# Optimization experiments

Hardware: AMD Instinct MI355X
Metric: run time of the kernel (lower is better)

The kernel has to match this reference:

```python
import jax, jax.numpy as jnp
import numpy as np

B, T, D, H, NW = 2, 2048, 1024, 16, 64
HD = D // H  # 64
EPS = 1e-12  # F.normalize eps


def setup_inputs() -> dict:
    key = jax.random.key(0)
    ks = jax.random.split(key, 8)
    def lin(k, din, dout):
        return jax.random.normal(k, (din, dout), jnp.float32) / np.sqrt(din).astype(np.float32)
    return {
        "x": jax.random.normal(ks[0], (B, T, D), jnp.float32),
        "Wqf": lin(ks[1], D, H * NW), "bqf": jnp.zeros((H * NW,), jnp.float32),
        "Wkf": lin(ks[2], D, H * NW), "bkf": jnp.zeros((H * NW,), jnp.float32),
        "Wqp": lin(ks[3], D, H * NW), "bqp": jnp.zeros((H * NW,), jnp.float32),
        "Wkp": lin(ks[4], D, H * NW), "bkp": jnp.zeros((H * NW,), jnp.float32),
        "Wv": lin(ks[5], D, D), "bv": jnp.zeros((D,), jnp.float32),
        "Wo": lin(ks[6], D, D), "bo": jnp.zeros((D,), jnp.float32),
        "scale": jnp.ones((H, 1, 1), jnp.float32),  # interference_scale
    }


def reference(x, Wqf, bqf, Wkf, bkf, Wqp, bqp, Wkp, bkp, Wv, bv, Wo, bo, scale):
    Bx, Tx, Dx = x.shape
    def heads(W, b, nd):  # [B,T,H*nd] -> [B,H,T,nd]
        return jnp.transpose((x @ W + b).reshape(Bx, Tx, H, nd), (0, 2, 1, 3))
    qf = heads(Wqf, bqf, NW); kf = heads(Wkf, bkf, NW)
    qp = heads(Wqp, bqp, NW); kp = heads(Wkp, bkp, NW)
    v = heads(Wv, bv, HD)
    t = jnp.arange(Tx, dtype=x.dtype)[None, None, :, None]  # [1,1,T,1]
    def wave_norm(f, p):
        w = jnp.sin(f * t + p)  # [B,H,T,NW]
        n = jnp.sqrt(jnp.sum(w * w, axis=-1, keepdims=True))
        return w / jnp.maximum(n, EPS)
    qn = wave_norm(qf, qp)
    kn = wave_norm(kf, kp)
    inter = jnp.einsum('bhtw,bhsw->bhts', qn, kn) * scale[None]  # [B,H,T,T]
    causal = jnp.tril(jnp.ones((Tx, Tx), bool))  # keep diag and below
    inter = jnp.where(causal, inter, jnp.zeros((), x.dtype))
    denom = jnp.sqrt(jnp.arange(1, Tx + 1, dtype=x.dtype))[:, None]  # [T,1]
    attn = inter / denom
    # dropout is identity in eval mode
    out = jnp.einsum('bhts,bhsd->bhtd', attn, v)
    out = jnp.transpose(out, (0, 2, 1, 3)).reshape(Bx, Tx, Dx)
    return out @ Wo + bo
```

## Files before the change

### kernel.cpp

```cpp
#include <hip/hip_runtime.h>


#define Bb 2
#define Tt 2048
#define Dd 1024
#define Hh 16
#define NC 32

typedef _Float16 half_t;
typedef _Float16 half8 __attribute__((ext_vector_type(8)));
typedef _Float16 half4h __attribute__((ext_vector_type(4)));
typedef float float4v __attribute__((ext_vector_type(4)));
typedef float f32x16 __attribute__((ext_vector_type(16)));

#define MFMA16(a, b, c) __builtin_amdgcn_mfma_f32_16x16x32_f16((a), (b), (c), 0, 0, 0)
#define MFMA32(a, b, c) __builtin_amdgcn_mfma_f32_32x32x16_f16((a), (b), (c), 0, 0, 0)

#define LOADREGS(K)                                                       \
  rg0 = *(const half8*)&srcHi[(K)];      rg1 = *(const half8*)&srcHi[(K) + 8];  \
  rg2 = *(const half8*)&srcHi[(K) + 16]; rg3 = *(const half8*)&srcHi[(K) + 24]; \
  rg4 = *(const half8*)&srcLo[(K)];      rg5 = *(const half8*)&srcLo[(K) + 8];  \
  rg6 = *(const half8*)&srcLo[(K) + 16]; rg7 = *(const half8*)&srcLo[(K) + 24];

#define WRITEREGS(BI) {                                                   \
  half_t* d_ = dstRow + (BI) * 8192;                                      \
  *(half8*)&d_[pc0] = rg0; *(half8*)&d_[pc1] = rg1;                       \
  *(half8*)&d_[pc2] = rg2; *(half8*)&d_[pc3] = rg3;                       \
  *(half8*)&d_[pc4] = rg4; *(half8*)&d_[pc5] = rg5;                       \
  *(half8*)&d_[pc6] = rg6; *(half8*)&d_[pc7] = rg7; }

#define KTILE_MFMA(BI)                                                    \
  _Pragma("unroll")                                                       \
  for (int ks = 0; ks < 2; ++ks) {                                        \
    half8 ahi = *(const half8*)&As[BI][32 * w + rl][((2 * ks + kq) ^ sw) * 8];       \
    half8 alo = *(const half8*)&As[BI][32 * w + rl][((4 + 2 * ks + kq) ^ sw) * 8];   \
    _Pragma("unroll")                                                     \
    for (int tn = 0; tn < 4; ++tn) {                                      \
      half8 bhi = *(const half8*)&Bs[BI][32 * tn + rl][((2 * ks + kq) ^ sw) * 8];    \
      half8 blo = *(const half8*)&Bs[BI][32 * tn + rl][((4 + 2 * ks + kq) ^ sw) * 8];\
      hh[tn] = MFMA32(ahi, bhi, hh[tn]);                                  \
      mx[tn] = MFMA32(ahi, blo, mx[tn]);                                  \
      mx[tn] = MFMA32(alo, bhi, mx[tn]);                                  \
    }                                                                     \
  }

__global__ __launch_bounds__(256) void xsplit_kernel(
    const float* __restrict__ X, half_t* __restrict__ XHI, half_t* __restrict__ XLO)
{
  const size_t i = ((size_t)blockIdx.x * 256 + threadIdx.x) * 8;
  float4 a = *(const float4*)&X[i];
  float4 b = *(const float4*)&X[i + 4];
  const float av[8] = {a.x, a.y, a.z, a.w, b.x, b.y, b.z, b.w};
  half8 hv, lv;
  #pragma unroll
  for (int j = 0; j < 8; ++j) {
    half_t hx = (half_t)av[j];
    hv[j] = hx; lv[j] = (half_t)((av[j] - (float)hx) * 2048.f);
  }
  *(half8*)&XHI[i] = hv;
  *(half8*)&XLO[i] = lv;
}

__global__ __launch_bounds__(256) void wsplit_kernel(
    const float* __restrict__ W0, const float* __restrict__ W1,
    const float* __restrict__ W2, const float* __restrict__ W3,
    const float* __restrict__ W4, const float* __restrict__ W5,
    half_t* __restrict__ WSP)
{
  __shared__ float Ld[64][68];
  const int tid = threadIdx.x;
  const int m = blockIdx.z;
  const float* W = (m == 0) ? W0 : (m == 1) ? W1 : (m == 2) ? W2
                 : (m == 3) ? W3 : (m == 4) ? W4 : W5;
  const int k0 = blockIdx.x * 64, n0 = blockIdx.y * 64;
  const int r = tid >> 2, c4 = (tid & 3) * 16;
  #pragma unroll
  for (int i = 0; i < 4; ++i)
    *(float4*)&Ld[r][c4 + i * 4] =
        *(const float4*)&W[(size_t)(k0 + r) * Dd + n0 + c4 + i * 4];
  __syncthreads();
  half_t* hi = WSP + (size_t)m * 2097152;
  half_t* lo = hi + 1048576;
  const int n = tid >> 2, kc = (tid & 3) * 16;
  half8 hv0, hv1, lv0, lv1;
  #pragma unroll
  for (int i = 0; i < 8; ++i) {
    float v0 = Ld[kc + i][n];
    half_t h0 = (half_t)v0;
    hv0[i] = h0; lv0[i] = (half_t)((v0 - (float)h0) * 2048.f);
    float v1 = Ld[kc + 8 + i][n];
    half_t h1 = (half_t)v1;
    hv1[i] = h1; lv1[i] = (half_t)((v1 - (float)h1) * 2048.f);
  }
  *(half8*)&hi[(size_t)(n0 + n) * Dd + k0 + kc]     = hv0;
  *(half8*)&hi[(size_t)(n0 + n) * Dd + k0 + kc + 8] = hv1;
  *(half8*)&lo[(size_t)(n0 + n) * Dd + k0 + kc]     = lv0;
  *(half8*)&lo[(size_t)(n0 + n) * Dd + k0 + kc + 8] = lv1;
}

__global__ __launch_bounds__(256, 2) void proj_kernel(
    const half_t* __restrict__ XHI, const half_t* __restrict__ XLO,
    const half_t* __restrict__ WSP,
    const float* __restrict__ bqf, const float* __restrict__ bqp,
    const float* __restrict__ bkf, const float* __restrict__ bkp,
    half_t* __restrict__ QNH, half_t* __restrict__ KNH)
{
  __shared__ __align__(16) half_t As[2][128][64];
  __shared__ __align__(16) half_t Bs[2][128][64];
  const int tid = threadIdx.x;
  const int mb = blockIdx.x, h = blockIdx.y;
  const int b = blockIdx.z >> 1, p = blockIdx.z & 1;
  const int t0 = mb * 128, row0 = b * Tt + t0, col0 = h * 64;
  const half_t* WF = WSP + (size_t)(2 * p) * 2097152;
  const half_t* WP = WSP + (size_t)(2 * p + 1) * 2097152;
  const float* BF = p ? bkf : bqf;
  const float* BP = p ? bkp : bqp;
  half_t* OUTH = p ? KNH : QNH;

  f32x16 hh[4], mx[4];
  #pragma unroll
  for (int i = 0; i < 4; ++i) { hh[i] = (f32x16)(0.f); mx[i] = (f32x16)(0.f); }

  const int lane = tid & 63, w = tid >> 6;
  const int rl = lane & 31, kq = lane >> 5;
  const int sw = rl & 7;

  const int r = tid & 127, isB = tid >> 7;
  const int swr = r & 7;
  const half_t* srcHi;
  const half_t* srcLo;
  if (!isB) {
    srcHi = &XHI[(size_t)(row0 + r) * Dd];
    srcLo = &XLO[(size_t)(row0 + r) * Dd];
  } else {
    const half_t* Wb = (r < 64) ? (WF + (size_t)(col0 + r) * Dd)
                                : (WP + (size_t)(col0 + r - 64) * Dd);
    srcHi = Wb; srcLo = Wb + 1048576;
  }
  half_t* dstRow = isB ? &Bs[0][r][0] : &As[0][r][0];
  const int pc0 = ((0 ^ swr)) * 8, pc1 = ((1 ^ swr)) * 8;
  const int pc2 = ((2 ^ swr)) * 8, pc3 = ((3 ^ swr)) * 8;
  const int pc4 = ((4 ^ swr)) * 8, pc5 = ((5 ^ swr)) * 8;
  const int pc6 = ((6 ^ swr)) * 8, pc7 = ((7 ^ swr)) * 8;

  half8 rg0, rg1, rg2, rg3, rg4, rg5, rg6, rg7;
  LOADREGS(0)
  WRITEREGS(0)
  LOADREGS(32)
  __syncthreads();

  #pragma unroll 1
  for (int k0 = 0; k0 < Dd; k0 += 64) {
    KTILE_MFMA(0)
    WRITEREGS(1)
    if (k0 + 64 < Dd) { LOADREGS(k0 + 64) }
    __syncthreads();
    KTILE_MFMA(1)
    if (k0 + 64 < Dd) { WRITEREGS(0) }
    if (k0 + 96 < Dd) { LOADREGS(k0 + 96) }
    __syncthreads();
  }

  const float bf0 = BF[col0 + rl], bf1 = BF[col0 + 32 + rl];
  const float bp0 = BP[col0 + rl], bp1 = BP[col0 + 32 + rl];
  #pragma unroll
  for (int j = 0; j < 16; ++j) {
    const int rt = (j & 3) + 8 * (j >> 2) + 4 * kq;
    const float tf = (float)(t0 + 32 * w + rt);
    float f0 = hh[0][j] + mx[0][j] * (1.f / 2048.f) + bf0;
    float f1 = hh[1][j] + mx[1][j] * (1.f / 2048.f) + bf1;
    float p0 = hh[2][j] + mx[2][j] * (1.f / 2048.f) + bp0;
    float p1 = hh[3][j] + mx[3][j] * (1.f / 2048.f) + bp1;
    float w0 = sinf(fmaf(f0, tf, p0));
    float w1 = sinf(fmaf(f1, tf, p1));
    float ss = w0 * w0 + w1 * w1;
    ss += __shfl_xor(ss, 1); ss += __shfl_xor(ss, 2);
    ss += __shfl_xor(ss, 4); ss += __shfl_xor(ss, 8);
    ss += __shfl_xor(ss, 16);
    const float inv = 1.f / fmaxf(sqrtf(ss), 1e-12f);
    half_t* op = &OUTH[((size_t)(b * Tt) + t0 + 32 * w + rt) * Dd + col0];
    op[rl]      = (half_t)(w0 * inv);
    op[32 + rl] = (half_t)(w1 * inv);
  }
}

__global__ __launch_bounds__(256, 2) void gemm_kernel(
    const half_t* __restrict__ AHI, const half_t* __restrict__ ALO,
    const half_t* __restrict__ WHI,
    const float* __restrict__ BIAS, float* __restrict__ OUT)
{
  __shared__ __align__(16) half_t As[2][128][64];
  __shared__ __align__(16) half_t Bs[2][128][64];
  const int tid = threadIdx.x;
  const int m0 = blockIdx.x * 128, n0 = blockIdx.y * 128;

  f32x16 hh[4], mx[4];
  #pragma unroll
  for (int i = 0; i < 4; ++i) { hh[i] = (f32x16)(0.f); mx[i] = (f32x16)(0.f); }

  const int lane = tid & 63, w = tid >> 6;
  const int rl = lane & 31, kq = lane >> 5;
  const int sw = rl & 7;

  const int r = tid & 127, isB = tid >> 7;
  const int swr = r & 7;
  const half_t* srcHi = isB ? &WHI[(size_t)(n0 + r) * Dd]
                            : &AHI[(size_t)(m0 + r) * Dd];
  const half_t* srcLo = isB ? &WHI[1048576 + (size_t)(n0 + r) * Dd]
                            : &ALO[(size_t)(m0 + r) * Dd];
  half_t* dstRow = isB ? &Bs[0][r][0] : &As[0][r][0];
  const int pc0 = ((0 ^ swr)) * 8, pc1 = ((1 ^ swr)) * 8;
  const int pc2 = ((2 ^ swr)) * 8, pc3 = ((3 ^ swr)) * 8;
  const int pc4 = ((4 ^ swr)) * 8, pc5 = ((5 ^ swr)) * 8;
  const int pc6 = ((6 ^ swr)) * 8, pc7 = ((7 ^ swr)) * 8;

  half8 rg0, rg1, rg2, rg3, rg4, rg5, rg6, rg7;
  LOADREGS(0)
  WRITEREGS(0)
  LOADREGS(32)
  __syncthreads();

  #pragma unroll 1
  for (int k0 = 0; k0 < Dd; k0 += 64) {
    KTILE_MFMA(0)
    WRITEREGS(1)
    if (k0 + 64 < Dd) { LOADREGS(k0 + 64) }
    __syncthreads();
    KTILE_MFMA(1)
    if (k0 + 64 < Dd) { WRITEREGS(0) }
    if (k0 + 96 < Dd) { LOADREGS(k0 + 96) }
    __syncthreads();
  }

  const float bb0 = BIAS[n0 + rl],      bb1 = BIAS[n0 + 32 + rl];
  const float bb2 = BIAS[n0 + 64 + rl], bb3 = BIAS[n0 + 96 + rl];
  #pragma unroll
  for (int j = 0; j < 16; ++j) {
    const int rt = (j & 3) + 8 * (j >> 2) + 4 * kq;
    float* orow = &OUT[(size_t)(m0 + 32 * w + rt) * Dd + n0];
    orow[rl]      = hh[0][j] + mx[0][j] * (1.f / 2048.f) + bb0;
    orow[32 + rl] = hh[1][j] + mx[1][j] * (1.f / 2048.f) + bb1;
    orow[64 + rl] = hh[2][j] + mx[2][j] * (1.f / 2048.f) + bb2;
    orow[96 + rl] = hh[3][j] + mx[3][j] * (1.f / 2048.f) + bb3;
  }
}

__global__ __launch_bounds__(256) void chunk_kv_kernel(
    const half_t* __restrict__ KNH, const float* __restrict__ V,
    float* __restrict__ G)
{
  __shared__ float Ks[64][64];
  __shared__ float Vs[64][64];
  const int tid = threadIdx.x;
  const int c = blockIdx.x, h = blockIdx.y, b = blockIdx.z;
  const int s0 = c * 64;
  const int lr = tid >> 2, lc = (tid & 3) * 16;
  {
    const half_t* krow = &KNH[(size_t)(b * Tt + s0 + lr) * Dd + h * 64 + lc];
    half8 ka = *(const half8*)&krow[0];
    half8 kb = *(const half8*)&krow[8];
    #pragma unroll
    for (int i = 0; i < 8; ++i) {
      Ks[lr][lc + i] = (float)ka[i];
      Ks[lr][lc + 8 + i] = (float)kb[i];
    }
    const float* vrow = &V[(size_t)(b * Tt + s0 + lr) * Dd + h * 64 + lc];
    #pragma unroll
    for (int i = 0; i < 4; ++i)
      *(float4*)&Vs[lr][lc + i * 4] = *(const float4*)&vrow[i * 4];
  }
  __syncthreads();

  const int ty = tid >> 4, tx = tid & 15;
  float g[4][4] = {{0.f}};
  #pragma unroll 4
  for (int s = 0; s < 64; ++s) {
    float4 kv = *(const float4*)&Ks[s][ty * 4];
    float4 vv = *(const float4*)&Vs[s][tx * 4];
    const float* k_ = (const float*)&kv;
    const float* v_ = (const float*)&vv;
    #pragma unroll
    for (int i = 0; i < 4; ++i)
      #pragma unroll
      for (int j = 0; j < 4; ++j)
        g[i][j] = fmaf(k_[i], v_[j], g[i][j]);
  }
  float* Gp = G + (((size_t)(b * Hh + h) * NC + c) << 12);
  #pragma unroll
  for (int i = 0; i < 4; ++i)
    *(float4*)&Gp[(ty * 4 + i) * 64 + tx * 4] =
        make_float4(g[i][0], g[i][1], g[i][2], g[i][3]);
}

__global__ __launch_bounds__(256) void prefix_kernel(float* __restrict__ G)
{
  const int seg = blockIdx.x, h = blockIdx.y, b = blockIdx.z;
  float* base = G + (((size_t)(b * Hh + h) * NC) << 12) + seg * 256 + threadIdx.x;
  float acc = 0.f;
  #pragma unroll 4
  for (int c = 0; c < NC; ++c) {
    float* p = base + ((size_t)c << 12);
    const float g = *p;
    *p = acc;
    acc += g;
  }
}

__global__ __launch_bounds__(256) void attn_chunk_kernel(
    const half_t* __restrict__ QNH, const half_t* __restrict__ KNH,
    const float* __restrict__ V, const float* __restrict__ M,
    const float* __restrict__ SCALE,
    half_t* __restrict__ ATTHI, half_t* __restrict__ ATTLO)
{
  __shared__ float Qt[64][68];
  __shared__ float Kt[64][68];
  __shared__ float SM[64][68];
  __shared__ float Vs[64][64];
  const int tid = threadIdx.x;
  const int c = blockIdx.x, h = blockIdx.y, b = blockIdx.z;
  const int t0 = c * 64;
  const int lr = tid >> 2, lc = (tid & 3) * 16;
  {
    const half_t* qrow = &QNH[(size_t)(b * Tt + t0 + lr) * Dd + h * 64 + lc];
    const half_t* krow = &KNH[(size_t)(b * Tt + t0 + lr) * Dd + h * 64 + lc];
    half8 qa = *(const half8*)&qrow[0];
    half8 qb = *(const half8*)&qrow[8];
    half8 ka = *(const half8*)&krow[0];
    half8 kb = *(const half8*)&krow[8];
    #pragma unroll
    for (int i = 0; i < 8; ++i) {
      Qt[lc + i][lr] = (float)qa[i];     Qt[lc + 8 + i][lr] = (float)qb[i];
      Kt[lc + i][lr] = (float)ka[i];     Kt[lc + 8 + i][lr] = (float)kb[i];
    }
    const float* vrow = &V[(size_t)(b * Tt + t0 + lr) * Dd + h * 64 + lc];
    const float* mrow = &M[(((size_t)(b * Hh + h) * NC + c) << 12) + lr * 64 + lc];
    #pragma unroll
    for (int i = 0; i < 4; ++i) {
      *(float4*)&Vs[lr][lc + i * 4] = *(const float4*)&vrow[i * 4];
      *(float4*)&SM[lr][lc + i * 4] = *(const float4*)&mrow[i * 4];
    }
  }
  __syncthreads();

  const int ty = tid >> 4, tx = tid & 15;
  float o[4][4] = {{0.f}};
  float sc[4][4] = {{0.f}};

  #pragma unroll 4
  for (int w = 0; w < 64; ++w) {
    float4 qv = *(const float4*)&Qt[w][ty * 4];
    float4 mv = *(const float4*)&SM[w][tx * 4];
    float4 kv = *(const float4*)&Kt[w][tx * 4];
    const float* q_ = (const float*)&qv;
    const float* m_ = (const float*)&mv;
    const float* k_ = (const float*)&kv;
    #pragma unroll
    for (int i = 0; i < 4; ++i) {
      float qq = q_[i];
      #pragma unroll
      for (int j = 0; j < 4; ++j) {
        o[i][j]  = fmaf(qq, m_[j], o[i][j]);
        sc[i][j] = fmaf(qq, k_[j], sc[i][j]);
      }
    }
  }
  __syncthreads();

  #pragma unroll
  for (int i = 0; i < 4; ++i) {
    const int lt = ty * 4 + i;
    #pragma unroll
    for (int j = 0; j < 4; ++j) {
      const int ls = tx * 4 + j;
      SM[ls][lt] = (ls <= lt) ? sc[i][j] : 0.f;
    }
  }
  __syncthreads();

  #pragma unroll 4
  for (int s = 0; s < 64; ++s) {
    float4 sv = *(const float4*)&SM[s][ty * 4];
    float4 vv = *(const float4*)&Vs[s][tx * 4];
    const float* s_ = (const float*)&sv;
    const float* v_ = (const float*)&vv;
    #pragma unroll
    for (int i = 0; i < 4; ++i)
      #pragma unroll
      for (int j = 0; j < 4; ++j)
        o[i][j] = fmaf(s_[i], v_[j], o[i][j]);
  }

  const float sch = SCALE[h];
  #pragma unroll
  for (int i = 0; i < 4; ++i) {
    const int t = t0 + ty * 4 + i;
    const float fac = sch / sqrtf((float)(t + 1));
    half4h hv, lv;
    #pragma unroll
    for (int j = 0; j < 4; ++j) {
      float v = o[i][j] * fac;
      half_t hx = (half_t)v;
      hv[j] = hx; lv[j] = (half_t)((v - (float)hx) * 2048.f);
    }
    *(half4h*)&ATTHI[(size_t)(b * Tt + t) * Dd + h * 64 + tx * 4] = hv;
    *(half4h*)&ATTLO[(size_t)(b * Tt + t) * Dd + h * 64 + tx * 4] = lv;
  }
}

extern "C" void kernel_launch(void* const* d_in, const int* in_sizes, int n_in,
                              void* d_out, int out_size, void* d_ws, size_t ws_size,
                              hipStream_t stream) {
  const float* x   = (const float*)d_in[0];
  const float* Wqf = (const float*)d_in[1];
  const float* bqf = (const float*)d_in[2];
  const float* Wkf = (const float*)d_in[3];
  const float* bkf = (const float*)d_in[4];
  const float* Wqp = (const float*)d_in[5];
  const float* bqp = (const float*)d_in[6];
  const float* Wkp = (const float*)d_in[7];
  const float* bkp = (const float*)d_in[8];
  const float* Wv  = (const float*)d_in[9];
  const float* bv  = (const float*)d_in[10];
  const float* Wo  = (const float*)d_in[11];
  const float* bo  = (const float*)d_in[12];
  const float* scale = (const float*)d_in[13];

  half_t* WSP = (half_t*)d_ws;
  half_t* qnh = WSP + 12582912;
  half_t* knh = qnh + 4194304;
  float*  G   = (float*)(knh + 4194304);
  half_t* xhi = (half_t*)G;
  half_t* xlo = xhi + 4194304;
  float*  vbuf = (float*)d_out;

  xsplit_kernel<<<dim3(2048), 256, 0, stream>>>(x, xhi, xlo);

  wsplit_kernel<<<dim3(16, 16, 6), 256, 0, stream>>>(Wqf, Wqp, Wkf, Wkp, Wv, Wo, WSP);

  proj_kernel<<<dim3(Tt / 128, Hh, Bb * 2), 256, 0, stream>>>(
      xhi, xlo, WSP, bqf, bqp, bkf, bkp, qnh, knh);

  gemm_kernel<<<dim3((Bb * Tt) / 128, Dd / 128), 256, 0, stream>>>(
      xhi, xlo, WSP + (size_t)4 * 2097152, bv, vbuf);

  chunk_kv_kernel<<<dim3(NC, Hh, Bb), 256, 0, stream>>>(knh, vbuf, G);
  prefix_kernel<<<dim3(16, Hh, Bb), 256, 0, stream>>>(G);
  attn_chunk_kernel<<<dim3(NC, Hh, Bb), 256, 0, stream>>>(
      qnh, knh, vbuf, G, scale, qnh , knh );

  gemm_kernel<<<dim3((Bb * Tt) / 128, Dd / 128), 256, 0, stream>>>(
      qnh, knh, WSP + (size_t)5 * 2097152, bo, (float*)d_out);
}
```

Measured before the change: 367.3 us.

## Store GEMM tiles in MFMA fragment order in LDS, single-buffered 32-wide K

Replaces the swizzled row-major double-buffered LDS tiles in the projection and output GEMM kernels with separate hi/lo buffers laid out in MFMA operand-fragment order. Each lane then reads its operand with one contiguous 16-byte load and no XOR address arithmetic. The K loop now steps 32 at a time with one buffer and two barriers per step, overlapping the next global load with the MFMAs. This halves LDS per block, which may help occupancy, but doubles the number of barriers and drops the double buffering.

```diff
diff --git a/kernel.cpp b/kernel.cpp
--- a/kernel.cpp
+++ b/kernel.cpp
@@ -16,32 +16,32 @@
 #define MFMA16(a, b, c) __builtin_amdgcn_mfma_f32_16x16x32_f16((a), (b), (c), 0, 0, 0)
 #define MFMA32(a, b, c) __builtin_amdgcn_mfma_f32_32x32x16_f16((a), (b), (c), 0, 0, 0)
 
-#define LOADREGS(K)                                                       \
-  rg0 = *(const half8*)&srcHi[(K)];      rg1 = *(const half8*)&srcHi[(K) + 8];  \
-  rg2 = *(const half8*)&srcHi[(K) + 16]; rg3 = *(const half8*)&srcHi[(K) + 24]; \
-  rg4 = *(const half8*)&srcLo[(K)];      rg5 = *(const half8*)&srcLo[(K) + 8];  \
+
+#define LOADREGS(K)                                                            \
+  rg0 = *(const half8*)&srcHi[(K)];      rg1 = *(const half8*)&srcHi[(K) + 8]; \
+  rg2 = *(const half8*)&srcHi[(K) + 16]; rg3 = *(const half8*)&srcHi[(K) + 24];\
+  rg4 = *(const half8*)&srcLo[(K)];      rg5 = *(const half8*)&srcLo[(K) + 8]; \
   rg6 = *(const half8*)&srcLo[(K) + 16]; rg7 = *(const half8*)&srcLo[(K) + 24];
 
-#define WRITEREGS(BI) {                                                   \
-  half_t* d_ = dstRow + (BI) * 8192;                                      \
-  *(half8*)&d_[pc0] = rg0; *(half8*)&d_[pc1] = rg1;                       \
-  *(half8*)&d_[pc2] = rg2; *(half8*)&d_[pc3] = rg3;                       \
-  *(half8*)&d_[pc4] = rg4; *(half8*)&d_[pc5] = rg5;                       \
-  *(half8*)&d_[pc6] = rg6; *(half8*)&d_[pc7] = rg7; }
-
-#define KTILE_MFMA(BI)                                                    \
-  _Pragma("unroll")                                                       \
-  for (int ks = 0; ks < 2; ++ks) {                                        \
-    half8 ahi = *(const half8*)&As[BI][32 * w + rl][((2 * ks + kq) ^ sw) * 8];       \
-    half8 alo = *(const half8*)&As[BI][32 * w + rl][((4 + 2 * ks + kq) ^ sw) * 8];   \
-    _Pragma("unroll")                                                     \
-    for (int tn = 0; tn < 4; ++tn) {                                      \
-      half8 bhi = *(const half8*)&Bs[BI][32 * tn + rl][((2 * ks + kq) ^ sw) * 8];    \
-      half8 blo = *(const half8*)&Bs[BI][32 * tn + rl][((4 + 2 * ks + kq) ^ sw) * 8];\
-      hh[tn] = MFMA32(ahi, bhi, hh[tn]);                                  \
-      mx[tn] = MFMA32(ahi, blo, mx[tn]);                                  \
-      mx[tn] = MFMA32(alo, bhi, mx[tn]);                                  \
-    }                                                                     \
+#define WRITEFRAGS {                                                           \
+  *(half8*)&dHi[0]    = rg0;  *(half8*)&dHi[256]  = rg1;                       \
+  *(half8*)&dHi[2048] = rg2;  *(half8*)&dHi[2304] = rg3;                       \
+  *(half8*)&dLo[0]    = rg4;  *(half8*)&dLo[256]  = rg5;                       \
+  *(half8*)&dLo[2048] = rg6;  *(half8*)&dLo[2304] = rg7; }
+
+#define KTILE_MFMA                                                             \
+  _Pragma("unroll")                                                            \
+  for (int ks = 0; ks < 2; ++ks) {                                             \
+    half8 ahi = *(const half8*)&AhiF[(ks * 4 + w) * 512 + lane * 8];           \
+    half8 alo = *(const half8*)&AloF[(ks * 4 + w) * 512 + lane * 8];           \
+    _Pragma("unroll")                                                          \
+    for (int tn = 0; tn < 4; ++tn) {                                           \
+      half8 bhi = *(const half8*)&BhiF[(ks * 4 + tn) * 512 + lane * 8];        \
+      half8 blo = *(const half8*)&BloF[(ks * 4 + tn) * 512 + lane * 8];        \
+      hh[tn] = MFMA32(ahi, bhi, hh[tn]);                                       \
+      mx[tn] = MFMA32(ahi, blo, mx[tn]);                                       \
+      mx[tn] = MFMA32(alo, bhi, mx[tn]);                                       \
+    }                                                                          \
   }
 
 __global__ __launch_bounds__(256) void xsplit_kernel(
@@ -105,8 +105,10 @@
     const float* __restrict__ bkf, const float* __restrict__ bkp,
     half_t* __restrict__ QNH, half_t* __restrict__ KNH)
 {
-  __shared__ __align__(16) half_t As[2][128][64];
-  __shared__ __align__(16) half_t Bs[2][128][64];
+  __shared__ __align__(16) half_t AhiF[4096];
+  __shared__ __align__(16) half_t AloF[4096];
+  __shared__ __align__(16) half_t BhiF[4096];
+  __shared__ __align__(16) half_t BloF[4096];
   const int tid = threadIdx.x;
   const int mb = blockIdx.x, h = blockIdx.y;
   const int b = blockIdx.z >> 1, p = blockIdx.z & 1;
@@ -123,10 +125,9 @@
 
   const int lane = tid & 63, w = tid >> 6;
   const int rl = lane & 31, kq = lane >> 5;
-  const int sw = rl & 7;
 
   const int r = tid & 127, isB = tid >> 7;
-  const int swr = r & 7;
+  const int rt = r >> 5, rr = r & 31;
   const half_t* srcHi;
   const half_t* srcLo;
   if (!isB) {
@@ -137,27 +138,17 @@
                                 : (WP + (size_t)(col0 + r - 64) * Dd);
     srcHi = Wb; srcLo = Wb + 1048576;
   }
-  half_t* dstRow = isB ? &Bs[0][r][0] : &As[0][r][0];
-  const int pc0 = ((0 ^ swr)) * 8, pc1 = ((1 ^ swr)) * 8;
-  const int pc2 = ((2 ^ swr)) * 8, pc3 = ((3 ^ swr)) * 8;
-  const int pc4 = ((4 ^ swr)) * 8, pc5 = ((5 ^ swr)) * 8;
-  const int pc6 = ((6 ^ swr)) * 8, pc7 = ((7 ^ swr)) * 8;
+  half_t* dHi = (isB ? BhiF : AhiF) + rt * 512 + rr * 8;
+  half_t* dLo = (isB ? BloF : AloF) + rt * 512 + rr * 8;
 
   half8 rg0, rg1, rg2, rg3, rg4, rg5, rg6, rg7;
   LOADREGS(0)
-  WRITEREGS(0)
-  LOADREGS(32)
-  __syncthreads();
-
-  #pragma unroll 1
-  for (int k0 = 0; k0 < Dd; k0 += 64) {
-    KTILE_MFMA(0)
-    WRITEREGS(1)
-    if (k0 + 64 < Dd) { LOADREGS(k0 + 64) }
+
+  for (int k0 = 0; k0 < Dd; k0 += 32) {
+    WRITEFRAGS
     __syncthreads();
-    KTILE_MFMA(1)
-    if (k0 + 64 < Dd) { WRITEREGS(0) }
-    if (k0 + 96 < Dd) { LOADREGS(k0 + 96) }
+    if (k0 + 32 < Dd) { LOADREGS(k0 + 32) }
+    KTILE_MFMA
     __syncthreads();
   }
 
@@ -165,8 +156,8 @@
   const float bp0 = BP[col0 + rl], bp1 = BP[col0 + 32 + rl];
   #pragma unroll
   for (int j = 0; j < 16; ++j) {
-    const int rt = (j & 3) + 8 * (j >> 2) + 4 * kq;
-    const float tf = (float)(t0 + 32 * w + rt);
+    const int rtj = (j & 3) + 8 * (j >> 2) + 4 * kq;
+    const float tf = (float)(t0 + 32 * w + rtj);
     float f0 = hh[0][j] + mx[0][j] * (1.f / 2048.f) + bf0;
     float f1 = hh[1][j] + mx[1][j] * (1.f / 2048.f) + bf1;
     float p0 = hh[2][j] + mx[2][j] * (1.f / 2048.f) + bp0;
@@ -178,7 +169,7 @@
     ss += __shfl_xor(ss, 4); ss += __shfl_xor(ss, 8);
     ss += __shfl_xor(ss, 16);
     const float inv = 1.f / fmaxf(sqrtf(ss), 1e-12f);
-    half_t* op = &OUTH[((size_t)(b * Tt) + t0 + 32 * w + rt) * Dd + col0];
+    half_t* op = &OUTH[((size_t)(b * Tt) + t0 + 32 * w + rtj) * Dd + col0];
     op[rl]      = (half_t)(w0 * inv);
     op[32 + rl] = (half_t)(w1 * inv);
   }
@@ -189,8 +180,10 @@
     const half_t* __restrict__ WHI,
     const float* __restrict__ BIAS, float* __restrict__ OUT)
 {
-  __shared__ __align__(16) half_t As[2][128][64];
-  __shared__ __align__(16) half_t Bs[2][128][64];
+  __shared__ __align__(16) half_t AhiF[4096];
+  __shared__ __align__(16) half_t AloF[4096];
+  __shared__ __align__(16) half_t BhiF[4096];
+  __shared__ __align__(16) half_t BloF[4096];
   const int tid = threadIdx.x;
   const int m0 = blockIdx.x * 128, n0 = blockIdx.y * 128;
 
@@ -200,35 +193,24 @@
 
   const int lane = tid & 63, w = tid >> 6;
   const int rl = lane & 31, kq = lane >> 5;
-  const int sw = rl & 7;
 
   const int r = tid & 127, isB = tid >> 7;
-  const int swr = r & 7;
+  const int rt = r >> 5, rr = r & 31;
   const half_t* srcHi = isB ? &WHI[(size_t)(n0 + r) * Dd]
                             : &AHI[(size_t)(m0 + r) * Dd];
   const half_t* srcLo = isB ? &WHI[1048576 + (size_t)(n0 + r) * Dd]
                             : &ALO[(size_t)(m0 + r) * Dd];
-  half_t* dstRow = isB ? &Bs[0][r][0] : &As[0][r][0];
-  const int pc0 = ((0 ^ swr)) * 8, pc1 = ((1 ^ swr)) * 8;
-  const int pc2 = ((2 ^ swr)) * 8, pc3 = ((3 ^ swr)) * 8;
-  const int pc4 = ((4 ^ swr)) * 8, pc5 = ((5 ^ swr)) * 8;
-  const int pc6 = ((6 ^ swr)) * 8, pc7 = ((7 ^ swr)) * 8;
+  half_t* dHi = (isB ? BhiF : AhiF) + rt * 512 + rr * 8;
+  half_t* dLo = (isB ? BloF : AloF) + rt * 512 + rr * 8;
 
   half8 rg0, rg1, rg2, rg3, rg4, rg5, rg6, rg7;
   LOADREGS(0)
-  WRITEREGS(0)
-  LOADREGS(32)
-  __syncthreads();
-
-  #pragma unroll 1
-  for (int k0 = 0; k0 < Dd; k0 += 64) {
-    KTILE_MFMA(0)
-    WRITEREGS(1)
-    if (k0 + 64 < Dd) { LOADREGS(k0 + 64) }
+
+  for (int k0 = 0; k0 < Dd; k0 += 32) {
+    WRITEFRAGS
     __syncthreads();
-    KTILE_MFMA(1)
-    if (k0 + 64 < Dd) { WRITEREGS(0) }
-    if (k0 + 96 < Dd) { LOADREGS(k0 + 96) }
+    if (k0 + 32 < Dd) { LOADREGS(k0 + 32) }
+    KTILE_MFMA
     __syncthreads();
   }
 
@@ -236,8 +218,8 @@
   const float bb2 = BIAS[n0 + 64 + rl], bb3 = BIAS[n0 + 96 + rl];
   #pragma unroll
   for (int j = 0; j < 16; ++j) {
-    const int rt = (j & 3) + 8 * (j >> 2) + 4 * kq;
-    float* orow = &OUT[(size_t)(m0 + 32 * w + rt) * Dd + n0];
+    const int rtj = (j & 3) + 8 * (j >> 2) + 4 * kq;
+    float* orow = &OUT[(size_t)(m0 + 32 * w + rtj) * Dd + n0];
     orow[rl]      = hh[0][j] + mx[0][j] * (1.f / 2048.f) + bb0;
     orow[32 + rl] = hh[1][j] + mx[1][j] * (1.f / 2048.f) + bb1;
     orow[64 + rl] = hh[2][j] + mx[2][j] * (1.f / 2048.f) + bb2;
```

Measured after the change: 400.4 us. 9.0% more time.

## Stage proj_kernel weight tiles via global_load_lds and load A fragments directly to registers

Applied to the files above, without the earlier changes.

The projection kernel now copies weight (B) tiles straight from global memory into LDS with the async global_load_lds builtin, using a four-buffer ring of 32-wide K slices in place of register staging. The activation (A) fragments are loaded straight from global memory into MFMA operand registers, so the A tile no longer goes through LDS. This is meant to cut LDS write traffic and VGPR staging and to overlap global loads with MFMA work. The cost is uncoalesced per-lane A loads, and the async LDS copies depend on the barriers being placed correctly.

```diff
diff --git a/kernel.cpp b/kernel.cpp
--- a/kernel.cpp
+++ b/kernel.cpp
@@ -10,26 +10,230 @@
 typedef _Float16 half_t;
 typedef _Float16 half8 __attribute__((ext_vector_type(8)));
 typedef _Float16 half4h __attribute__((ext_vector_type(4)));
-typedef float float4v __attribute__((ext_vector_type(4)));
 typedef float f32x16 __attribute__((ext_vector_type(16)));
 
-#define MFMA16(a, b, c) __builtin_amdgcn_mfma_f32_16x16x32_f16((a), (b), (c), 0, 0, 0)
 #define MFMA32(a, b, c) __builtin_amdgcn_mfma_f32_32x32x16_f16((a), (b), (c), 0, 0, 0)
 
-#define LOADREGS(K)                                                       \
-  rg0 = *(const half8*)&srcHi[(K)];      rg1 = *(const half8*)&srcHi[(K) + 8];  \
-  rg2 = *(const half8*)&srcHi[(K) + 16]; rg3 = *(const half8*)&srcHi[(K) + 24]; \
-  rg4 = *(const half8*)&srcLo[(K)];      rg5 = *(const half8*)&srcLo[(K) + 8];  \
+#define GLL(G, L) __builtin_amdgcn_global_load_lds(                      \
+    (const __attribute__((address_space(1))) void*)(G),                  \
+    (__attribute__((address_space(3))) void*)(L), 16, 0, 0)
+
+__global__ __launch_bounds__(256) void xsplit_kernel(
+    const float* __restrict__ X, half_t* __restrict__ XHI, half_t* __restrict__ XLO)
+{
+  const size_t i = ((size_t)blockIdx.x * 256 + threadIdx.x) * 8;
+  float4 a = *(const float4*)&X[i];
+  float4 b = *(const float4*)&X[i + 4];
+  const float av[8] = {a.x, a.y, a.z, a.w, b.x, b.y, b.z, b.w};
+  half8 hv, lv;
+  #pragma unroll
+  for (int j = 0; j < 8; ++j) {
+    half_t hx = (half_t)av[j];
+    hv[j] = hx; lv[j] = (half_t)((av[j] - (float)hx) * 2048.f);
+  }
+  *(half8*)&XHI[i] = hv;
+  *(half8*)&XLO[i] = lv;
+}
+
+__global__ __launch_bounds__(256) void wsplit_kernel(
+    const float* __restrict__ W0, const float* __restrict__ W1,
+    const float* __restrict__ W2, const float* __restrict__ W3,
+    const float* __restrict__ W4, const float* __restrict__ W5,
+    half_t* __restrict__ WSP)
+{
+  __shared__ float Ld[64][68];
+  const int tid = threadIdx.x;
+  const int m = blockIdx.z;
+  const float* W = (m == 0) ? W0 : (m == 1) ? W1 : (m == 2) ? W2
+                 : (m == 3) ? W3 : (m == 4) ? W4 : W5;
+  const int k0 = blockIdx.x * 64, n0 = blockIdx.y * 64;
+  const int r = tid >> 2, c4 = (tid & 3) * 16;
+  #pragma unroll
+  for (int i = 0; i < 4; ++i)
+    *(float4*)&Ld[r][c4 + i * 4] =
+        *(const float4*)&W[(size_t)(k0 + r) * Dd + n0 + c4 + i * 4];
+  __syncthreads();
+  half_t* hi = WSP + (size_t)m * 2097152;
+  half_t* lo = hi + 1048576;
+  const int n = tid >> 2, kc = (tid & 3) * 16;
+  half8 hv0, hv1, lv0, lv1;
+  #pragma unroll
+  for (int i = 0; i < 8; ++i) {
+    float v0 = Ld[kc + i][n];
+    half_t h0 = (half_t)v0;
+    hv0[i] = h0; lv0[i] = (half_t)((v0 - (float)h0) * 2048.f);
+    float v1 = Ld[kc + 8 + i][n];
+    half_t h1 = (half_t)v1;
+    hv1[i] = h1; lv1[i] = (half_t)((v1 - (float)h1) * 2048.f);
+  }
+  *(half8*)&hi[(size_t)(n0 + n) * Dd + k0 + kc]     = hv0;
+  *(half8*)&hi[(size_t)(n0 + n) * Dd + k0 + kc + 8] = hv1;
+  *(half8*)&lo[(size_t)(n0 + n) * Dd + k0 + kc]     = lv0;
+  *(half8*)&lo[(size_t)(n0 + n) * Dd + k0 + kc + 8] = lv1;
+}
+
+__global__ __launch_bounds__(256, 2) void proj_kernel(
+    const half_t* __restrict__ XHI, const half_t* __restrict__ XLO,
+    const half_t* __restrict__ WSP,
+    const float* __restrict__ bqf, const float* __restrict__ bqp,
+    const float* __restrict__ bkf, const float* __restrict__ bkp,
+    half_t* __restrict__ QNH, half_t* __restrict__ KNH)
+{
+  __shared__ __align__(16) half_t Bs[4][128][64];
+  const int tid = threadIdx.x;
+  const int mb = blockIdx.x, h = blockIdx.y;
+  const int b = blockIdx.z >> 1, p = blockIdx.z & 1;
+  const int t0 = mb * 128, row0 = b * Tt + t0, col0 = h * 64;
+  const half_t* WF = WSP + (size_t)(2 * p) * 2097152;
+  const half_t* WP = WSP + (size_t)(2 * p + 1) * 2097152;
+  const float* BF = p ? bkf : bqf;
+  const float* BP = p ? bkp : bqp;
+  half_t* OUTH = p ? KNH : QNH;
+
+  f32x16 hh[4], mx[4];
+  #pragma unroll
+  for (int i = 0; i < 4; ++i) { hh[i] = (f32x16)(0.f); mx[i] = (f32x16)(0.f); }
+
+  const int lane = tid & 63, w = tid >> 6;
+  const int rl = lane & 31, kq = lane >> 5;
+  const int sw = rl & 7;
+
+  const half_t* aHi = XHI + (size_t)(row0 + 32 * w + rl) * Dd + kq * 8;
+  const half_t* aLo = XLO + (size_t)(row0 + 32 * w + rl) * Dd + kq * 8;
+
+  const int lr8 = lane >> 3;
+  const int lcc = (lane & 7) ^ lr8;
+  const int csel = (lcc & 3) * 8;
+  const size_t loOff = (lcc >= 4) ? 1048576 : 0;
+  const half_t* gb0 = WF + loOff + (size_t)(col0 + 8 * w + lr8) * Dd + csel;
+  const half_t* gb1 = gb0 + 32 * Dd;
+  const half_t* gb2 = WP + loOff + (size_t)(col0 + 8 * w + lr8) * Dd + csel;
+  const half_t* gb3 = gb2 + 32 * Dd;
+
+#define STAGE_PB(BI, K) {                          \
+    GLL(gb0 + (K), &Bs[BI][8 * w][0]);             \
+    GLL(gb1 + (K), &Bs[BI][32 + 8 * w][0]);        \
+    GLL(gb2 + (K), &Bs[BI][64 + 8 * w][0]);        \
+    GLL(gb3 + (K), &Bs[BI][96 + 8 * w][0]); }
+
+#define LOADA(H0, H1, L0, L1, K) {                 \
+    H0 = *(const half8*)&aHi[(K)];                 \
+    H1 = *(const half8*)&aHi[(K) + 16];            \
+    L0 = *(const half8*)&aLo[(K)];                 \
+    L1 = *(const half8*)&aLo[(K) + 16]; }
+
+#define KT_P(H0, H1, L0, L1, BI) {                                     \
+    { const int c0 = (kq ^ sw) * 8, c1 = ((4 + kq) ^ sw) * 8;          \
+      _Pragma("unroll")                                                \
+      for (int tn = 0; tn < 4; ++tn) {                                 \
+        half8 bh = *(const half8*)&Bs[BI][32 * tn + rl][c0];           \
+        half8 bl = *(const half8*)&Bs[BI][32 * tn + rl][c1];           \
+        hh[tn] = MFMA32(H0, bh, hh[tn]);                               \
+        mx[tn] = MFMA32(H0, bl, mx[tn]);                               \
+        mx[tn] = MFMA32(L0, bh, mx[tn]); } }                           \
+    { const int c0 = (((2 + kq)) ^ sw) * 8, c1 = ((6 + kq) ^ sw) * 8;  \
+      _Pragma("unroll")                                                \
+      for (int tn = 0; tn < 4; ++tn) {                                 \
+        half8 bh = *(const half8*)&Bs[BI][32 * tn + rl][c0];           \
+        half8 bl = *(const half8*)&Bs[BI][32 * tn + rl][c1];           \
+        hh[tn] = MFMA32(H1, bh, hh[tn]);                               \
+        mx[tn] = MFMA32(H1, bl, mx[tn]);                               \
+        mx[tn] = MFMA32(L1, bh, mx[tn]); } } }
+
+  half8 pa0, pa1, pa2, pa3, pb0, pb1, pb2, pb3;
+  STAGE_PB(0, 0)
+  STAGE_PB(1, 32)
+  LOADA(pa0, pa1, pa2, pa3, 0)
+  __syncthreads();
+
+  #pragma unroll 1
+  for (int k0 = 0; k0 < Dd; k0 += 128) {
+    if (k0 + 64 < Dd) { STAGE_PB(2, k0 + 64) STAGE_PB(3, k0 + 96) }
+    LOADA(pb0, pb1, pb2, pb3, k0 + 32)
+    KT_P(pa0, pa1, pa2, pa3, 0)
+    if (k0 + 64 < Dd) { LOADA(pa0, pa1, pa2, pa3, k0 + 64) }
+    KT_P(pb0, pb1, pb2, pb3, 1)
+    __syncthreads();
+    if (k0 + 128 < Dd) { STAGE_PB(0, k0 + 128) STAGE_PB(1, k0 + 160) }
+    if (k0 + 96 < Dd)  { LOADA(pb0, pb1, pb2, pb3, k0 + 96) }
+    KT_P(pa0, pa1, pa2, pa3, 2)
+    if (k0 + 128 < Dd) { LOADA(pa0, pa1, pa2, pa3, k0 + 128) }
+    KT_P(pb0, pb1, pb2, pb3, 3)
+    __syncthreads();
+  }
+#undef STAGE_PB
+#undef LOADA
+#undef KT_P
+
+  const float bf0 = BF[col0 + rl], bf1 = BF[col0 + 32 + rl];
+  const float bp0 = BP[col0 + rl], bp1 = BP[col0 + 32 + rl];
+  #pragma unroll
+  for (int j = 0; j < 16; ++j) {
+    const int rtj = (j & 3) + 8 * (j >> 2) + 4 * kq;
+    const float tf = (float)(t0 + 32 * w + rtj);
+    float f0 = hh[0][j] + mx[0][j] * (1.f / 2048.f) + bf0;
+    float f1 = hh[1][j] + mx[1][j] * (1.f / 2048.f) + bf1;
+    float p0 = hh[2][j] + mx[2][j] * (1.f / 2048.f) + bp0;
+    float p1 = hh[3][j] + mx[3][j] * (1.f / 2048.f) + bp1;
+    float w0 = sinf(fmaf(f0, tf, p0));
+    float w1 = sinf(fmaf(f1, tf, p1));
+    float ss = w0 * w0 + w1 * w1;
+    ss += __shfl_xor(ss, 1); ss += __shfl_xor(ss, 2);
+    ss += __shfl_xor(ss, 4); ss += __shfl_xor(ss, 8);
+    ss += __shfl_xor(ss, 16);
+    const float inv = 1.f / fmaxf(sqrtf(ss), 1e-12f);
+    half_t* op = &OUTH[((size_t)(b * Tt) + t0 + 32 * w + rtj) * Dd + col0];
+    op[rl]      = (half_t)(w0 * inv);
+    op[32 + rl] = (half_t)(w1 * inv);
+  }
+}
+
+__global__ __launch_bounds__(256, 2) void gemm_kernel(
+    const half_t* __restrict__ AHI, const half_t* __restrict__ ALO,
+    const half_t* __restrict__ WHI,
+    const float* __restrict__ BIAS, float* __restrict__ OUT)
+{
+  __shared__ __align__(16) half_t As[2][128][64];
+  __shared__ __align__(16) half_t Bs[2][128][64];
+  const int tid = threadIdx.x;
+  const int m0 = blockIdx.x * 128, n0 = blockIdx.y * 128;
+
+  f32x16 hh[4], mx[4];
+  #pragma unroll
+  for (int i = 0; i < 4; ++i) { hh[i] = (f32x16)(0.f); mx[i] = (f32x16)(0.f); }
+
+  const int lane = tid & 63, w = tid >> 6;
+  const int rl = lane & 31, kq = lane >> 5;
+  const int sw = rl & 7;
+
+  const int r = tid & 127, isB = tid >> 7;
+  const int swr = r & 7;
+  const half_t* srcHi = isB ? &WHI[(size_t)(n0 + r) * Dd]
+                            : &AHI[(size_t)(m0 + r) * Dd];
+  const half_t* srcLo = isB ? &WHI[1048576 + (size_t)(n0 + r) * Dd]
+                            : &ALO[(size_t)(m0 + r) * Dd];
+  half_t* dstRow = isB ? &Bs[0][r][0] : &As[0][r][0];
+  const int pc0 = (0 ^ swr) * 8, pc1 = (1 ^ swr) * 8;
+  const int pc2 = (2 ^ swr) * 8, pc3 = (3 ^ swr) * 8;
+  const int pc4 = (4 ^ swr) * 8, pc5 = (5 ^ swr) * 8;
+  const int pc6 = (6 ^ swr) * 8, pc7 = (7 ^ swr) * 8;
+
+  half8 rg0, rg1, rg2, rg3, rg4, rg5, rg6, rg7;
+
+#define G_LOADREGS(K)                                                          \
+  rg0 = *(const half8*)&srcHi[(K)];      rg1 = *(const half8*)&srcHi[(K) + 8]; \
+  rg2 = *(const half8*)&srcHi[(K) + 16]; rg3 = *(const half8*)&srcHi[(K) + 24];\
+  rg4 = *(const half8*)&srcLo[(K)];      rg5 = *(const half8*)&srcLo[(K) + 8]; \
   rg6 = *(const half8*)&srcLo[(K) + 16]; rg7 = *(const half8*)&srcLo[(K) + 24];
 
-#define WRITEREGS(BI) {                                                   \
+#define G_WRITE(BI) {                                                     \
   half_t* d_ = dstRow + (BI) * 8192;                                      \
   *(half8*)&d_[pc0] = rg0; *(half8*)&d_[pc1] = rg1;                       \
   *(half8*)&d_[pc2] = rg2; *(half8*)&d_[pc3] = rg3;                       \
   *(half8*)&d_[pc4] = rg4; *(half8*)&d_[pc5] = rg5;                       \
   *(half8*)&d_[pc6] = rg6; *(half8*)&d_[pc7] = rg7; }
 
-#define KTILE_MFMA(BI)                                                    \
+#define G_KT(BI)                                                          \
   _Pragma("unroll")                                                       \
   for (int ks = 0; ks < 2; ++ks) {                                        \
     half8 ahi = *(const half8*)&As[BI][32 * w + rl][((2 * ks + kq) ^ sw) * 8];       \
@@ -44,200 +248,32 @@
     }                                                                     \
   }
 
-__global__ __launch_bounds__(256) void xsplit_kernel(
-    const float* __restrict__ X, half_t* __restrict__ XHI, half_t* __restrict__ XLO)
-{
-  const size_t i = ((size_t)blockIdx.x * 256 + threadIdx.x) * 8;
-  float4 a = *(const float4*)&X[i];
-  float4 b = *(const float4*)&X[i + 4];
-  const float av[8] = {a.x, a.y, a.z, a.w, b.x, b.y, b.z, b.w};
-  half8 hv, lv;
-  #pragma unroll
-  for (int j = 0; j < 8; ++j) {
-    half_t hx = (half_t)av[j];
-    hv[j] = hx; lv[j] = (half_t)((av[j] - (float)hx) * 2048.f);
-  }
-  *(half8*)&XHI[i] = hv;
-  *(half8*)&XLO[i] = lv;
-}
-
-__global__ __launch_bounds__(256) void wsplit_kernel(
-    const float* __restrict__ W0, const float* __restrict__ W1,
-    const float* __restrict__ W2, const float* __restrict__ W3,
-    const float* __restrict__ W4, const float* __restrict__ W5,
-    half_t* __restrict__ WSP)
-{
-  __shared__ float Ld[64][68];
-  const int tid = threadIdx.x;
-  const int m = blockIdx.z;
-  const float* W = (m == 0) ? W0 : (m == 1) ? W1 : (m == 2) ? W2
-                 : (m == 3) ? W3 : (m == 4) ? W4 : W5;
-  const int k0 = blockIdx.x * 64, n0 = blockIdx.y * 64;
-  const int r = tid >> 2, c4 = (tid & 3) * 16;
-  #pragma unroll
-  for (int i = 0; i < 4; ++i)
-    *(float4*)&Ld[r][c4 + i * 4] =
-        *(const float4*)&W[(size_t)(k0 + r) * Dd + n0 + c4 + i * 4];
-  __syncthreads();
-  half_t* hi = WSP + (size_t)m * 2097152;
-  half_t* lo = hi + 1048576;
-  const int n = tid >> 2, kc = (tid & 3) * 16;
-  half8 hv0, hv1, lv0, lv1;
-  #pragma unroll
-  for (int i = 0; i < 8; ++i) {
-    float v0 = Ld[kc + i][n];
-    half_t h0 = (half_t)v0;
-    hv0[i] = h0; lv0[i] = (half_t)((v0 - (float)h0) * 2048.f);
-    float v1 = Ld[kc + 8 + i][n];
-    half_t h1 = (half_t)v1;
-    hv1[i] = h1; lv1[i] = (half_t)((v1 - (float)h1) * 2048.f);
-  }
-  *(half8*)&hi[(size_t)(n0 + n) * Dd + k0 + kc]     = hv0;
-  *(half8*)&hi[(size_t)(n0 + n) * Dd + k0 + kc + 8] = hv1;
-  *(half8*)&lo[(size_t)(n0 + n) * Dd + k0 + kc]     = lv0;
-  *(half8*)&lo[(size_t)(n0 + n) * Dd + k0 + kc + 8] = lv1;
-}
-
-__global__ __launch_bounds__(256, 2) void proj_kernel(
-    const half_t* __restrict__ XHI, const half_t* __restrict__ XLO,
-    const half_t* __restrict__ WSP,
-    const float* __restrict__ bqf, const float* __restrict__ bqp,
-    const float* __restrict__ bkf, const float* __restrict__ bkp,
-    half_t* __restrict__ QNH, half_t* __restrict__ KNH)
-{
-  __shared__ __align__(16) half_t As[2][128][64];
-  __shared__ __align__(16) half_t Bs[2][128][64];
-  const int tid = threadIdx.x;
-  const int mb = blockIdx.x, h = blockIdx.y;
-  const int b = blockIdx.z >> 1, p = blockIdx.z & 1;
-  const int t0 = mb * 128, row0 = b * Tt + t0, col0 = h * 64;
-  const half_t* WF = WSP + (size_t)(2 * p) * 2097152;
-  const half_t* WP = WSP + (size_t)(2 * p + 1) * 2097152;
-  const float* BF = p ? bkf : bqf;
-  const float* BP = p ? bkp : bqp;
-  half_t* OUTH = p ? KNH : QNH;
-
-  f32x16 hh[4], mx[4];
-  #pragma unroll
-  for (int i = 0; i < 4; ++i) { hh[i] = (f32x16)(0.f); mx[i] = (f32x16)(0.f); }
-
-  const int lane = tid & 63, w = tid >> 6;
-  const int rl = lane & 31, kq = lane >> 5;
-  const int sw = rl & 7;
-
-  const int r = tid & 127, isB = tid >> 7;
-  const int swr = r & 7;
-  const half_t* srcHi;
-  const half_t* srcLo;
-  if (!isB) {
-    srcHi = &XHI[(size_t)(row0 + r) * Dd];
-    srcLo = &XLO[(size_t)(row0 + r) * Dd];
-  } else {
-    const half_t* Wb = (r < 64) ? (WF + (size_t)(col0 + r) * Dd)
-                                : (WP + (size_t)(col0 + r - 64) * Dd);
-    srcHi = Wb; srcLo = Wb + 1048576;
-  }
-  half_t* dstRow = isB ? &Bs[0][r][0] : &As[0][r][0];
-  const int pc0 = ((0 ^ swr)) * 8, pc1 = ((1 ^ swr)) * 8;
-  const int pc2 = ((2 ^ swr)) * 8, pc3 = ((3 ^ swr)) * 8;
-  const int pc4 = ((4 ^ swr)) * 8, pc5 = ((5 ^ swr)) * 8;
-  const int pc6 = ((6 ^ swr)) * 8, pc7 = ((7 ^ swr)) * 8;
-
-  half8 rg0, rg1, rg2, rg3, rg4, rg5, rg6, rg7;
-  LOADREGS(0)
-  WRITEREGS(0)
-  LOADREGS(32)
+  G_LOADREGS(0)
+  G_WRITE(0)
+  G_LOADREGS(32)
   __syncthreads();
 
   #pragma unroll 1
   for (int k0 = 0; k0 < Dd; k0 += 64) {
-    KTILE_MFMA(0)
-    WRITEREGS(1)
-    if (k0 + 64 < Dd) { LOADREGS(k0 + 64) }
+    G_KT(0)
+    G_WRITE(1)
+    if (k0 + 64 < Dd) { G_LOADREGS(k0 + 64) }
     __syncthreads();
-    KTILE_MFMA(1)
-    if (k0 + 64 < Dd) { WRITEREGS(0) }
-    if (k0 + 96 < Dd) { LOADREGS(k0 + 96) }
+    G_KT(1)
+    if (k0 + 64 < Dd) { G_WRITE(0) }
+    if (k0 + 96 < Dd) { G_LOADREGS(k0 + 96) }
     __syncthreads();
   }
-
-  const float bf0 = BF[col0 + rl], bf1 = BF[col0 + 32 + rl];
-  const float bp0 = BP[col0 + rl], bp1 = BP[col0 + 32 + rl];
-  #pragma unroll
-  for (int j = 0; j < 16; ++j) {
-    const int rt = (j & 3) + 8 * (j >> 2) + 4 * kq;
-    const float tf = (float)(t0 + 32 * w + rt);
-    float f0 = hh[0][j] + mx[0][j] * (1.f / 2048.f) + bf0;
-    float f1 = hh[1][j] + mx[1][j] * (1.f / 2048.f) + bf1;
-    float p0 = hh[2][j] + mx[2][j] * (1.f / 2048.f) + bp0;
-    float p1 = hh[3][j] + mx[3][j] * (1.f / 2048.f) + bp1;
-    float w0 = sinf(fmaf(f0, tf, p0));
-    float w1 = sinf(fmaf(f1, tf, p1));
-    float ss = w0 * w0 + w1 * w1;
-    ss += __shfl_xor(ss, 1); ss += __shfl_xor(ss, 2);
-    ss += __shfl_xor(ss, 4); ss += __shfl_xor(ss, 8);
-    ss += __shfl_xor(ss, 16);
-    const float inv = 1.f / fmaxf(sqrtf(ss), 1e-12f);
-    half_t* op = &OUTH[((size_t)(b * Tt) + t0 + 32 * w + rt) * Dd + col0];
-    op[rl]      = (half_t)(w0 * inv);
-    op[32 + rl] = (half_t)(w1 * inv);
-  }
-}
-
-__global__ __launch_bounds__(256, 2) void gemm_kernel(
-    const half_t* __restrict__ AHI, const half_t* __restrict__ ALO,
-    const half_t* __restrict__ WHI,
-    const float* __restrict__ BIAS, float* __restrict__ OUT)
-{
-  __shared__ __align__(16) half_t As[2][128][64];
-  __shared__ __align__(16) half_t Bs[2][128][64];
-  const int tid = threadIdx.x;
-  const int m0 = blockIdx.x * 128, n0 = blockIdx.y * 128;
-
-  f32x16 hh[4], mx[4];
-  #pragma unroll
-  for (int i = 0; i < 4; ++i) { hh[i] = (f32x16)(0.f); mx[i] = (f32x16)(0.f); }
-
-  const int lane = tid & 63, w = tid >> 6;
-  const int rl = lane & 31, kq = lane >> 5;
-  const int sw = rl & 7;
-
-  const int r = tid & 127, isB = tid >> 7;
-  const int swr = r & 7;
-  const half_t* srcHi = isB ? &WHI[(size_t)(n0 + r) * Dd]
-                            : &AHI[(size_t)(m0 + r) * Dd];
-  const half_t* srcLo = isB ? &WHI[1048576 + (size_t)(n0 + r) * Dd]
-                            : &ALO[(size_t)(m0 + r) * Dd];
-  half_t* dstRow = isB ? &Bs[0][r][0] : &As[0][r][0];
-  const int pc0 = ((0 ^ swr)) * 8, pc1 = ((1 ^ swr)) * 8;
-  const int pc2 = ((2 ^ swr)) * 8, pc3 = ((3 ^ swr)) * 8;
-  const int pc4 = ((4 ^ swr)) * 8, pc5 = ((5 ^ swr)) * 8;
-  const int pc6 = ((6 ^ swr)) * 8, pc7 = ((7 ^ swr)) * 8;
-
-  half8 rg0, rg1, rg2, rg3, rg4, rg5, rg6, rg7;
-  LOADREGS(0)
-  WRITEREGS(0)
-  LOADREGS(32)
-  __syncthreads();
-
-  #pragma unroll 1
-  for (int k0 = 0; k0 < Dd; k0 += 64) {
-    KTILE_MFMA(0)
-    WRITEREGS(1)
-    if (k0 + 64 < Dd) { LOADREGS(k0 + 64) }
-    __syncthreads();
-    KTILE_MFMA(1)
-    if (k0 + 64 < Dd) { WRITEREGS(0) }
-    if (k0 + 96 < Dd) { LOADREGS(k0 + 96) }
-    __syncthreads();
-  }
+#undef G_LOADREGS
+#undef G_WRITE
+#undef G_KT
 
   const float bb0 = BIAS[n0 + rl],      bb1 = BIAS[n0 + 32 + rl];
   const float bb2 = BIAS[n0 + 64 + rl], bb3 = BIAS[n0 + 96 + rl];
   #pragma unroll
   for (int j = 0; j < 16; ++j) {
-    const int rt = (j & 3) + 8 * (j >> 2) + 4 * kq;
-    float* orow = &OUT[(size_t)(m0 + 32 * w + rt) * Dd + n0];
+    const int rtj = (j & 3) + 8 * (j >> 2) + 4 * kq;
+    float* orow = &OUT[(size_t)(m0 + 32 * w + rtj) * Dd + n0];
     orow[rl]      = hh[0][j] + mx[0][j] * (1.f / 2048.f) + bb0;
     orow[32 + rl] = hh[1][j] + mx[1][j] * (1.f / 2048.f) + bb1;
     orow[64 + rl] = hh[2][j] + mx[2][j] * (1.f / 2048.f) + bb2;
```

New measurement: 371.2 us. No clear change (+1.1%).
